# Optimization experiments

Hardware: AMD Instinct MI355X
Metric: run time of the kernel (lower is better)

The kernel has to match this reference:

```python
import jax, jax.numpy as jnp
import numpy as np

N_WAY = 5
N_SHOT = 25
N_SUPPORT = N_WAY * N_SHOT  # 125
N_QUERY = 2048
D = 8192
C_REG = 0.1        # default C_reg of MetaOptNetHead_SVM_CS
MAX_ITER = 20      # default maxIter of QPFunction
SIGMA = 0.1        # centering parameter of the interior-point iteration


def setup_inputs() -> dict:
    key = jax.random.key(0)
    k1, k2, k3 = jax.random.split(key, 3)
    query = jax.random.normal(k1, (N_QUERY, D), dtype=jnp.float32)
    support = jax.random.normal(k2, (N_SUPPORT, D), dtype=jnp.float32)
    support_labels = jax.random.randint(k3, (N_SUPPORT,), 0, N_WAY, dtype=jnp.int32)
    scale = jnp.ones((1,), dtype=jnp.float32)  # nn.Parameter([1.0])
    return {
        "query": query,
        "support": support,
        "support_labels": support_labels,
        "n_way": N_WAY,
        "n_shot": N_SHOT,
        "scale": scale,
    }


def _solve_qp(G, e, h, A, b):
    """Solve min_z 0.5 z^T G z + e^T z  s.t.  z <= h (C = I),  A z = b.

    Primal-dual infeasible-start interior-point method with MAX_ITER fixed
    Newton steps (the jax analogue of qpth's QPFunction(maxIter=20)).
    Shapes: G (B,n,n), e (B,n), h (B,n), A (B,p,n), b (B,p).
    """
    B, n = e.shape
    p = b.shape[1]
    m = n  # C = I -> one inequality per variable
    At = jnp.swapaxes(A, 1, 2)                      # (B,n,p)
    zero_pp = jnp.zeros((B, p, p), dtype=G.dtype)
    A_row = jnp.concatenate([A, zero_pp], axis=2)   # (B,p,n+p), constant

    z = jnp.zeros_like(e)
    s = jnp.ones_like(h)
    lam = jnp.ones_like(h)
    nu = jnp.zeros_like(b)

    def frac_to_boundary(x, dx):
        # largest alpha in (0,1] keeping x + alpha*dx > 0
        ratio = jnp.where(dx < 0, -x / jnp.where(dx < 0, dx, -1.0), jnp.inf)
        return jnp.min(ratio, axis=1)

    def step(carry, _):
        z, s, lam, nu = carry
        Gz = jnp.einsum('bij,bj->bi', G, z)
        r1 = Gz + e + lam + jnp.einsum('bpi,bp->bi', A, nu)   # dual residual (C^T lam = lam)
        r2 = z + s - h                                         # primal ineq residual
        r4 = jnp.einsum('bpi,bi->bp', A, z) - b                # primal eq residual
        mu = SIGMA * jnp.sum(s * lam, axis=1, keepdims=True) / m
        r3 = lam * s - mu                                      # perturbed complementarity
        # Reduced KKT system: (G + diag(lam/s)) dz + A^T dnu = rhs1 ; A dz = -r4
        H = G + jax.vmap(jnp.diag)(lam / s)                    # (B,n,n)
        rhs1 = -(r1 + (lam * r2 - r3) / s)                     # (B,n)
        K = jnp.concatenate(
            [jnp.concatenate([H, At], axis=2), A_row], axis=1)  # (B,n+p,n+p)
        rhs = jnp.concatenate([rhs1, -r4], axis=1)             # (B,n+p)
        sol = jnp.linalg.solve(K, rhs[..., None])[..., 0]
        dz, dnu = sol[:, :n], sol[:, n:]
        ds = -r2 - dz
        dlam = (-r3 - lam * ds) / s
        alpha = jnp.minimum(
            1.0, 0.99 * jnp.minimum(frac_to_boundary(s, ds),
                                    frac_to_boundary(lam, dlam)))[:, None]
        return (z + alpha * dz, s + alpha * ds,
                lam + alpha * dlam, nu + alpha * dnu), None

    (z, s, lam, nu), _ = jax.lax.scan(step, (z, s, lam, nu), None, length=MAX_ITER)
    return z


def _svm_cs_head(query, support, support_labels, n_way):
    support_b = support[None]            # (1, ns, d) -- head unsqueezes batch dim
    query_b = query[None]                # (1, nq, d)
    B, ns, _ = support_b.shape
    f32 = jnp.float32

    # Gram matrix of support, then kron with I_{n_way} (batched_kronecker == jnp.kron)
    K = jnp.einsum('bnd,bmd->bnm', support_b, support_b)            # (B,ns,ns)
    eye_w = jnp.eye(n_way, dtype=f32)
    G = jax.vmap(lambda k: jnp.kron(k, eye_w))(K)                    # (B,ns*nw,ns*nw)
    G = G + jnp.eye(n_way * ns, dtype=f32)[None]

    y1h = jax.nn.one_hot(support_labels, n_way, dtype=f32).reshape(B, ns * n_way)
    e = -y1h
    h = C_REG * y1h
    A = jnp.kron(jnp.eye(ns, dtype=f32), jnp.ones((1, n_way), f32))[None]  # (1,ns,ns*nw)
    b = jnp.zeros((B, ns), f32)

    qp_sol = _solve_qp(G, e, h, A, b)                                # (B, ns*nw)

    compat = jnp.einsum('bnd,bqd->bnq', support_b, query_b)          # (B,ns,nq)
    qp3 = qp_sol.reshape(B, ns, n_way)
    # logits[b,q,w] = sum_s qp3[b,s,w] * compat[b,s,q]
    logits = jnp.einsum('bsw,bsq->bqw', qp3, compat)                 # (B,nq,nw)
    num_sv = jnp.sum(jnp.any(qp3 > 0.001, axis=2))                   # support-vector count
    return logits, num_sv


def reference(query, support, support_labels, n_way, n_shot, scale):
    logits, num_sv = _svm_cs_head(query, support, support_labels, n_way)
    return scale * logits, num_sv
```

## Files before the change

### kernel.cpp

```cpp
#include <hip/hip_runtime.h>

#define NS   125
#define NW   5
#define NQ   2048
#define DD   8192
#define CREG 0.1f
#define PGD_ITERS 10

#define OFF_PART  0
#define OFF_K     1000000
#define OFF_QP3   1016000
#define OFF_W     1017000

#define NPART     64

__global__ __launch_bounds__(256, 2) void gram192(const float* __restrict__ support,
                                                  float* __restrict__ part) {
    __shared__ __align__(16) float As[64][132];
    __shared__ __align__(16) float Bs[64][132];
    const int tid = threadIdx.x;
    const int qsel = blockIdx.x % 3;
    const int c    = blockIdx.x / 3;
    const int qy = (qsel == 2) ? 1 : 0;
    const int qz = (qsel == 0) ? 0 : 1;
    const int d0 = c * 128;
    const int sy0 = qy * 64, sz0 = qz * 64;

#pragma unroll
    for (int it = 0; it < 8; ++it) {
        int idx = it * 256 + tid;
        int sl = idx >> 5, d4 = idx & 31;
        int sa = sy0 + sl, sb = sz0 + sl;
        float4 va = (sa < NS) ? *(const float4*)&support[(size_t)sa * DD + d0 + d4 * 4]
                              : make_float4(0.f, 0.f, 0.f, 0.f);
        float4 vb = (sb < NS) ? *(const float4*)&support[(size_t)sb * DD + d0 + d4 * 4]
                              : make_float4(0.f, 0.f, 0.f, 0.f);
        *(float4*)&As[sl][d4 * 4] = va;
        *(float4*)&Bs[sl][d4 * 4] = vb;
    }
    __syncthreads();

    const int tx = tid & 15, ty = tid >> 4;
    float acc[4][4];
#pragma unroll
    for (int i = 0; i < 4; i++)
#pragma unroll
        for (int j = 0; j < 4; j++) acc[i][j] = 0.f;

#pragma unroll 4
    for (int d4 = 0; d4 < 32; ++d4) {
        float4 a4[4], b4[4];
#pragma unroll
        for (int i = 0; i < 4; i++) a4[i] = *(const float4*)&As[tx + 16 * i][d4 * 4];
#pragma unroll
        for (int j = 0; j < 4; j++) b4[j] = *(const float4*)&Bs[ty + 16 * j][d4 * 4];
#pragma unroll
        for (int i = 0; i < 4; i++)
#pragma unroll
            for (int j = 0; j < 4; j++)
                acc[i][j] += a4[i].x * b4[j].x + a4[i].y * b4[j].y
                           + a4[i].z * b4[j].z + a4[i].w * b4[j].w;
    }

    float* dst = part + (size_t)c * (NS * NS);
#pragma unroll
    for (int i = 0; i < 4; i++) {
        int gi = sy0 + tx + 16 * i;
        if (gi >= NS) continue;
#pragma unroll
        for (int j = 0; j < 4; j++) {
            int gj = sz0 + ty + 16 * j;
            if (gj < NS) dst[gi * NS + gj] = acc[i][j];
        }
    }
}

__global__ __launch_bounds__(256) void kreduce(const float* __restrict__ part,
                                               float* __restrict__ Kg) {
    int t = blockIdx.x * 256 + threadIdx.x;
    if (t < NS * NS) {
        int i = t / NS, j = t - i * NS;
        int src = (i >= 64 && j < 64) ? (j * NS + i) : t;
        float s = 0.f;
#pragma unroll 8
        for (int c = 0; c < NPART; ++c) s += part[(size_t)c * (NS * NS) + src];
        Kg[t] = s;
    }
}

__global__ __launch_bounds__(256) void qp_solve(const float* __restrict__ Kg,
                                                const int* __restrict__ labels,
                                                float* __restrict__ qp3,
                                                float* __restrict__ outNumSv) {
    __shared__ float red2[2][128 * 25];
    __shared__ float rsx[2];
    __shared__ int   svc;

    const int tid  = threadIdx.x;
    const int w    = tid >> 6;
    const int lane = tid & 63;
    const int c0   = w * 32;
    const int r0   = lane, r1 = lane + 64;

    float kr0[32], kr1[32];
#pragma unroll
    for (int j = 0; j < 32; ++j) {
        const int col = c0 + j;
        const bool cv = (col < NS);
        kr0[j] = cv ? Kg[col * NS + r0] : 0.f;
        kr1[j] = (cv && r1 < NS) ? Kg[col * NS + r1] : 0.f;
    }
    if (tid == 0) svc = 0;
    float rsum0 = 0.f, rsum1 = 0.f;
#pragma unroll
    for (int j = 0; j < 32; ++j) { rsum0 += fabsf(kr0[j]); rsum1 += fabsf(kr1[j]); }
    red2[0][r0 * 25 + w * 5] = rsum0;
    red2[0][r1 * 25 + w * 5] = rsum1;
    __syncthreads();
    const int prw = w * 64 + lane;
    if (w < 2) {
        const float* rr = &red2[0][prw * 25];
        float t = (prw < NS) ? rr[0] + rr[5] + rr[10] + rr[15] : 0.f;
#pragma unroll
        for (int off = 32; off; off >>= 1) t = fmaxf(t, __shfl_xor(t, off));
        if (lane == 0) rsx[w] = t;
    }
    __syncthreads();
    const float eta = 1.9f / (fmaxf(rsx[0], rsx[1]) + 1.0f);
    const int pr   = c0 + lane;
    const bool act = (lane < 32) && (pr < NS);
    const int lab  = act ? labels[pr] : 0;
    float z[NW] = {0.f, 0.f, 0.f, 0.f, 0.f};

    for (int it = 0; it < PGD_ITERS; ++it) {
        const int p = it & 1;
        float acc0[NW] = {0.f, 0.f, 0.f, 0.f, 0.f};
        float acc1[NW] = {0.f, 0.f, 0.f, 0.f, 0.f};
#pragma unroll
        for (int j = 0; j < 32; ++j) {
            float zj[NW];
#pragma unroll
            for (int a = 0; a < NW; a++)
                zj[a] = __uint_as_float(__builtin_amdgcn_readlane(__float_as_uint(z[a]), j));
            const float k0 = kr0[j], k1 = kr1[j];
#pragma unroll
            for (int a = 0; a < NW; a++) {
                acc0[a] = fmaf(k0, zj[a], acc0[a]);
                acc1[a] = fmaf(k1, zj[a], acc1[a]);
            }
        }
        {
            float* b0 = &red2[p][r0 * 25 + w * 5];
            b0[0] = acc0[0]; b0[1] = acc0[1]; b0[2] = acc0[2]; b0[3] = acc0[3]; b0[4] = acc0[4];
            float* b1 = &red2[p][r1 * 25 + w * 5];
            b1[0] = acc1[0]; b1[1] = acc1[1]; b1[2] = acc1[2]; b1[3] = acc1[3]; b1[4] = acc1[4];
        }
        __syncthreads();
        if (act) {
            const float* rr = &red2[p][pr * 25];
            float v[NW], h[NW];
#pragma unroll
            for (int a = 0; a < NW; a++) {
                float kz = rr[a] + rr[5 + a] + rr[10 + a] + rr[15 + a];
                float g = kz + z[a] - ((a == lab) ? 1.f : 0.f);
                v[a] = z[a] - eta * g;
                h[a] = (a == lab) ? CREG : 0.f;
            }
            float tau = fmaxf(fmaxf(fmaxf(v[0], v[1]), fmaxf(v[2], v[3])), v[4]);
#pragma unroll
            for (int nn = 0; nn < 7; ++nn) {
                float g = 0.f, nf = 0.f;
#pragma unroll
                for (int a = 0; a < NW; a++) {
                    float d = v[a] - tau;
                    bool fr = (d <= h[a]);
                    g += fr ? d : h[a];
                    nf += fr ? 1.f : 0.f;
                }
                float rnf = (nf > 4.5f) ? 0.2f
                          : (nf > 3.5f) ? 0.25f
                          : (nf > 2.5f) ? (1.f / 3.f)
                          : (nf > 1.5f) ? 0.5f : 1.f;
                tau += g * rnf;
            }
#pragma unroll
            for (int a = 0; a < NW; a++)
                z[a] = fminf(v[a] - tau, h[a]);
        }
    }

    if (act) {
        float m = fmaxf(fmaxf(fmaxf(z[0], z[1]), fmaxf(z[2], z[3])), z[4]);
        if (m > 0.001f) atomicAdd(&svc, 1);
#pragma unroll
        for (int a = 0; a < NW; a++) qp3[pr * NW + a] = z[a];
    }
    __syncthreads();
    if (tid == 0) *outNumSv = (float)svc;
}

__global__ __launch_bounds__(256) void w_kernel(const float* __restrict__ support,
                                                const float* __restrict__ qp3,
                                                float* __restrict__ W) {
    __shared__ float q3[NS * NW];
    __shared__ float red[4 * 64 * NW];
    const int tid = threadIdx.x;
    for (int i = tid; i < NS * NW; i += 256) q3[i] = qp3[i];
    __syncthreads();
    const int ld = tid & 63;
    const int sq = tid >> 6;
    const int d  = blockIdx.x * 64 + ld;
    const int s0 = sq * 32;
    const int s1 = (sq == 3) ? NS : (s0 + 32);
    float acc[NW] = {0.f, 0.f, 0.f, 0.f, 0.f};
#pragma unroll 4
    for (int s = s0; s < s1; ++s) {
        float sv = support[(size_t)s * DD + d];
#pragma unroll
        for (int a = 0; a < NW; a++) acc[a] += sv * q3[s * NW + a];
    }
    float* rr = &red[tid * NW];
#pragma unroll
    for (int a = 0; a < NW; a++) rr[a] = acc[a];
    __syncthreads();
    if (sq == 0) {
#pragma unroll
        for (int a = 0; a < NW; a++) {
            float s = red[(0 * 64 + ld) * NW + a] + red[(1 * 64 + ld) * NW + a]
                    + red[(2 * 64 + ld) * NW + a] + red[(3 * 64 + ld) * NW + a];
            W[(size_t)a * DD + d] = s;
        }
    }
}

__global__ __launch_bounds__(512) void logits8w(const float* __restrict__ query,
                                                const float* __restrict__ W,
                                                const float* __restrict__ scale,
                                                float* __restrict__ out) {
    __shared__ float red[8][8][NW];
    const int tid = threadIdx.x;
    const int wave = tid >> 6, lane = tid & 63;
    const int q0 = blockIdx.x * 8;
    const int v0 = wave * 256;
    const float4* W4 = (const float4*)W;
    const float4* q4 = (const float4*)query;
    const float sc = scale[0];

    float acc[8][NW];
#pragma unroll
    for (int k = 0; k < 8; k++)
#pragma unroll
        for (int a = 0; a < NW; a++) acc[k][a] = 0.f;

    for (int it = 0; it < 4; ++it) {
        const int dv = v0 + it * 64 + lane;
        float4 qv[8];
#pragma unroll
        for (int k = 0; k < 8; k++) qv[k] = q4[(size_t)(q0 + k) * (DD / 4) + dv];
#pragma unroll
        for (int a = 0; a < NW; a++) {
            float4 wv = W4[a * (DD / 4) + dv];
#pragma unroll
            for (int k = 0; k < 8; k++)
                acc[k][a] += qv[k].x * wv.x + qv[k].y * wv.y
                           + qv[k].z * wv.z + qv[k].w * wv.w;
        }
    }
#pragma unroll
    for (int off = 32; off; off >>= 1) {
#pragma unroll
        for (int k = 0; k < 8; k++)
#pragma unroll
            for (int a = 0; a < NW; a++) acc[k][a] += __shfl_xor(acc[k][a], off);
    }
    if (lane == 0) {
#pragma unroll
        for (int k = 0; k < 8; k++)
#pragma unroll
            for (int a = 0; a < NW; a++) red[wave][k][a] = acc[k][a];
    }
    __syncthreads();
    if (tid < 8 * NW) {
        const int ql = tid / NW, a = tid % NW;
        float s = 0.f;
#pragma unroll
        for (int wv = 0; wv < 8; ++wv) s += red[wv][ql][a];
        out[(q0 + ql) * NW + a] = sc * s;
    }
}

extern "C" void kernel_launch(void* const* d_in, const int* in_sizes, int n_in,
                              void* d_out, int out_size, void* d_ws, size_t ws_size,
                              hipStream_t stream) {
    const float* query   = (const float*)d_in[0];
    const float* support = (const float*)d_in[1];
    const int*   labels  = (const int*)d_in[2];
    const float* scale   = (const float*)d_in[5];
    float* out = (float*)d_out;
    float* ws  = (float*)d_ws;

    float* part = ws + OFF_PART;
    float* Kg   = ws + OFF_K;
    float* qp3  = ws + OFF_QP3;
    float* W    = ws + OFF_W;

    hipLaunchKernelGGL(gram192, dim3(192), dim3(256), 0, stream, support, part);
    hipLaunchKernelGGL(kreduce, dim3((NS * NS + 255) / 256), dim3(256), 0, stream, part, Kg);
    hipLaunchKernelGGL(qp_solve, dim3(1), dim3(256), 0, stream, Kg, labels, qp3, out + NQ * NW);
    hipLaunchKernelGGL(w_kernel, dim3(DD / 64), dim3(256), 0, stream, support, qp3, W);
    hipLaunchKernelGGL(logits8w, dim3(NQ / 8), dim3(512), 0, stream, query, W, scale, out);
}
```

Before: 157.4 us.

## Run QP iterations in a single wavefront with K staged in LDS

The projected-gradient QP solve now stages the full 125x125 Gram matrix in padded shared memory and runs every iteration inside one 64-lane wavefront. Each lane owns two rows, and the K·z product is done with readlane broadcasts, so the per-iteration cross-wave LDS reduction and __syncthreads are gone. The support-vector count is now done with ballot/popcount instead of a shared atomic. In exchange, one wave does four times the FMA work per iteration and reads K from LDS rather than from registers.

```diff
diff --git a/kernel.cpp b/kernel.cpp
--- a/kernel.cpp
+++ b/kernel.cpp
@@ -13,6 +13,7 @@
 #define OFF_W     1017000
 
 #define NPART     64
+#define KP        129
 
 __global__ __launch_bounds__(256, 2) void gram192(const float* __restrict__ support,
                                                   float* __restrict__ part) {
@@ -92,77 +93,71 @@
                                                 const int* __restrict__ labels,
                                                 float* __restrict__ qp3,
                                                 float* __restrict__ outNumSv) {
-    __shared__ float red2[2][128 * 25];
-    __shared__ float rsx[2];
-    __shared__ int   svc;
-
-    const int tid  = threadIdx.x;
-    const int w    = tid >> 6;
-    const int lane = tid & 63;
-    const int c0   = w * 32;
-    const int r0   = lane, r1 = lane + 64;
-
-    float kr0[32], kr1[32];
-#pragma unroll
-    for (int j = 0; j < 32; ++j) {
-        const int col = c0 + j;
-        const bool cv = (col < NS);
-        kr0[j] = cv ? Kg[col * NS + r0] : 0.f;
-        kr1[j] = (cv && r1 < NS) ? Kg[col * NS + r1] : 0.f;
-    }
-    if (tid == 0) svc = 0;
+    __shared__ float Ks[128 * KP];
+    const int tid = threadIdx.x;
+
+    for (int idx = tid; idx < NS * NS; idx += 256) {
+        int r = idx / NS, j = idx - r * NS;
+        Ks[r * KP + j] = Kg[idx];
+    }
+    for (int idx = tid; idx < 3 * NS; idx += 256) {
+        int r = 125 + idx / NS, j = idx % NS;
+        Ks[r * KP + j] = 0.f;
+    }
+    __syncthreads();
+    if (tid >= 64) return;
+
+    const int l  = tid;
+    const int r0 = l, r1 = l + 64;
+    const bool v1 = (r1 < NS);
+    const int lab0 = labels[r0];
+    const int lab1 = v1 ? labels[r1] : 0;
+    const float* K0 = &Ks[r0 * KP];
+    const float* K1 = &Ks[r1 * KP];
+
     float rsum0 = 0.f, rsum1 = 0.f;
-#pragma unroll
-    for (int j = 0; j < 32; ++j) { rsum0 += fabsf(kr0[j]); rsum1 += fabsf(kr1[j]); }
-    red2[0][r0 * 25 + w * 5] = rsum0;
-    red2[0][r1 * 25 + w * 5] = rsum1;
-    __syncthreads();
-    const int prw = w * 64 + lane;
-    if (w < 2) {
-        const float* rr = &red2[0][prw * 25];
-        float t = (prw < NS) ? rr[0] + rr[5] + rr[10] + rr[15] : 0.f;
-#pragma unroll
-        for (int off = 32; off; off >>= 1) t = fmaxf(t, __shfl_xor(t, off));
-        if (lane == 0) rsx[w] = t;
-    }
-    __syncthreads();
-    const float eta = 1.9f / (fmaxf(rsx[0], rsx[1]) + 1.0f);
-    const int pr   = c0 + lane;
-    const bool act = (lane < 32) && (pr < NS);
-    const int lab  = act ? labels[pr] : 0;
-    float z[NW] = {0.f, 0.f, 0.f, 0.f, 0.f};
+#pragma unroll 5
+    for (int j = 0; j < NS; ++j) { rsum0 += fabsf(K0[j]); rsum1 += fabsf(K1[j]); }
+    float m = fmaxf(rsum0, rsum1);
+#pragma unroll
+    for (int off = 32; off; off >>= 1) m = fmaxf(m, __shfl_xor(m, off));
+    const float eta = 1.9f / (m + 1.0f);
+
+    float z0[NW] = {0.f, 0.f, 0.f, 0.f, 0.f};
+    float z1[NW] = {0.f, 0.f, 0.f, 0.f, 0.f};
 
     for (int it = 0; it < PGD_ITERS; ++it) {
-        const int p = it & 1;
-        float acc0[NW] = {0.f, 0.f, 0.f, 0.f, 0.f};
-        float acc1[NW] = {0.f, 0.f, 0.f, 0.f, 0.f};
-#pragma unroll
-        for (int j = 0; j < 32; ++j) {
-            float zj[NW];
-#pragma unroll
-            for (int a = 0; a < NW; a++)
-                zj[a] = __uint_as_float(__builtin_amdgcn_readlane(__float_as_uint(z[a]), j));
-            const float k0 = kr0[j], k1 = kr1[j];
+        float kz0[NW] = {0.f, 0.f, 0.f, 0.f, 0.f};
+        float kz1[NW] = {0.f, 0.f, 0.f, 0.f, 0.f};
+#pragma unroll
+        for (int j = 0; j < 64; ++j) {
+            const float k0 = K0[j], k1 = K1[j];
 #pragma unroll
             for (int a = 0; a < NW; a++) {
-                acc0[a] = fmaf(k0, zj[a], acc0[a]);
-                acc1[a] = fmaf(k1, zj[a], acc1[a]);
+                float zj = __uint_as_float(__builtin_amdgcn_readlane(__float_as_uint(z0[a]), j));
+                kz0[a] = fmaf(k0, zj, kz0[a]);
+                kz1[a] = fmaf(k1, zj, kz1[a]);
             }
         }
-        {
-            float* b0 = &red2[p][r0 * 25 + w * 5];
-            b0[0] = acc0[0]; b0[1] = acc0[1]; b0[2] = acc0[2]; b0[3] = acc0[3]; b0[4] = acc0[4];
-            float* b1 = &red2[p][r1 * 25 + w * 5];
-            b1[0] = acc1[0]; b1[1] = acc1[1]; b1[2] = acc1[2]; b1[3] = acc1[3]; b1[4] = acc1[4];
-        }
-        __syncthreads();
-        if (act) {
-            const float* rr = &red2[p][pr * 25];
+#pragma unroll
+        for (int j = 64; j < NS; ++j) {
+            const float k0 = K0[j], k1 = K1[j];
+#pragma unroll
+            for (int a = 0; a < NW; a++) {
+                float zj = __uint_as_float(__builtin_amdgcn_readlane(__float_as_uint(z1[a]), j - 64));
+                kz0[a] = fmaf(k0, zj, kz0[a]);
+                kz1[a] = fmaf(k1, zj, kz1[a]);
+            }
+        }
+#pragma unroll
+        for (int row = 0; row < 2; ++row) {
+            float* z  = row ? z1 : z0;
+            float* kz = row ? kz1 : kz0;
+            const int lab = row ? lab1 : lab0;
             float v[NW], h[NW];
 #pragma unroll
             for (int a = 0; a < NW; a++) {
-                float kz = rr[a] + rr[5 + a] + rr[10 + a] + rr[15 + a];
-                float g = kz + z[a] - ((a == lab) ? 1.f : 0.f);
+                float g = kz[a] + z[a] - ((a == lab) ? 1.f : 0.f);
                 v[a] = z[a] - eta * g;
                 h[a] = (a == lab) ? CREG : 0.f;
             }
@@ -184,19 +179,21 @@
                 tau += g * rnf;
             }
 #pragma unroll
-            for (int a = 0; a < NW; a++)
-                z[a] = fminf(v[a] - tau, h[a]);
-        }
-    }
-
-    if (act) {
-        float m = fmaxf(fmaxf(fmaxf(z[0], z[1]), fmaxf(z[2], z[3])), z[4]);
-        if (m > 0.001f) atomicAdd(&svc, 1);
-#pragma unroll
-        for (int a = 0; a < NW; a++) qp3[pr * NW + a] = z[a];
-    }
-    __syncthreads();
-    if (tid == 0) *outNumSv = (float)svc;
+            for (int a = 0; a < NW; a++) z[a] = fminf(v[a] - tau, h[a]);
+        }
+    }
+
+    float m0 = fmaxf(fmaxf(fmaxf(z0[0], z0[1]), fmaxf(z0[2], z0[3])), z0[4]);
+    float m1 = fmaxf(fmaxf(fmaxf(z1[0], z1[1]), fmaxf(z1[2], z1[3])), z1[4]);
+    unsigned long long b0 = __ballot(m0 > 0.001f);
+    unsigned long long b1 = __ballot(v1 && (m1 > 0.001f));
+#pragma unroll
+    for (int a = 0; a < NW; a++) qp3[r0 * NW + a] = z0[a];
+    if (v1) {
+#pragma unroll
+        for (int a = 0; a < NW; a++) qp3[r1 * NW + a] = z1[a];
+    }
+    if (l == 0) *outNumSv = (float)(__popcll(b0) + __popcll(b1));
 }
 
 __global__ __launch_bounds__(256) void w_kernel(const float* __restrict__ support,
```

New measurement: 336.6 us. +113.9%, slower.
